# Kernel optimization log

Measured on AMD Instinct MI355X. Metric: run time of the kernel, lower is better.

Reference implementation:

```python
import jax, jax.numpy as jnp
import numpy as np

HEADS, CH = 10, 78          # GATv2Conv(78, 78, heads=10), concat=True -> 780
NUM_GRAPHS = 512            # from hardcoded (512 - 1) batch constant in forward
NEG_SLOPE = 0.2             # PyG GATv2 default


def _add_self_loops(edge_index, num_nodes):
    ar = jnp.arange(num_nodes, dtype=edge_index.dtype)
    loops = jnp.stack([ar, ar])
    return jnp.concatenate([edge_index, loops], axis=1)


def _gatv2_conv(x, edge_index, Wl, Wr, att_a, b_gat):
    # PyG GATv2Conv: e_ij = a^T LeakyReLU(W_l x_j + W_r x_i), softmax over j per i
    N = x.shape[0]
    ei = _add_self_loops(edge_index, N)
    src, dst = ei[0], ei[1]
    xl = (x @ Wl).reshape(N, HEADS, CH)  # source transform
    xr = (x @ Wr).reshape(N, HEADS, CH)  # target transform
    e = jax.nn.leaky_relu(xl[src] + xr[dst], NEG_SLOPE)      # [E, H, C]
    logits = jnp.einsum('ehc,hc->eh', e, att_a)              # [E, H]
    m = jax.ops.segment_max(logits, dst, num_segments=N)     # per-dst max
    p = jnp.exp(logits - m[dst])
    denom = jax.ops.segment_sum(p, dst, num_segments=N)
    alpha = p / denom[dst]                                   # [E, H]
    out = jax.ops.segment_sum(alpha[:, :, None] * xl[src], dst, num_segments=N)
    return out.reshape(N, HEADS * CH) + b_gat


def _gcn_conv(x, edge_index, W, b):
    # PyG GCNConv with self-loops and symmetric normalization
    N = x.shape[0]
    ei = _add_self_loops(edge_index, N)
    src, dst = ei[0], ei[1]
    deg = jax.ops.segment_sum(jnp.ones_like(dst, dtype=x.dtype), dst, num_segments=N)
    dinv = jnp.where(deg > 0, jax.lax.rsqrt(deg), 0.0)
    norm = dinv[src] * dinv[dst]                             # [E]
    h = x @ W
    return jax.ops.segment_sum(norm[:, None] * h[src], dst, num_segments=N) + b


def _pool_max_mean(x, batch):
    # global_max_pool and global_mean_pool over graph ids
    mx = jax.ops.segment_max(x, batch, num_segments=NUM_GRAPHS)
    mx = jnp.where(jnp.isfinite(mx), mx, 0.0)
    s = jax.ops.segment_sum(x, batch, num_segments=NUM_GRAPHS)
    cnt = jax.ops.segment_sum(jnp.ones((x.shape[0],), x.dtype), batch, num_segments=NUM_GRAPHS)
    mn = s / jnp.maximum(cnt, 1.0)[:, None]
    return jnp.concatenate([mx, mn], axis=1)


def setup_inputs() -> dict:
    key = jax.random.key(0)
    ks = jax.random.split(key, 13)
    N, E = 16384, 262144
    s = 0.05
    return {
        'x': jax.random.normal(ks[0], (N, 78), jnp.float32),
        'edge_index': jax.random.randint(ks[1], (2, E), 0, N, dtype=jnp.int32),
        'batch': jnp.sort(jax.random.randint(ks[2], (N,), 0, NUM_GRAPHS, dtype=jnp.int32)),
        'Wl': jax.random.normal(ks[3], (78, 780), jnp.float32) * s,
        'Wr': jax.random.normal(ks[4], (78, 780), jnp.float32) * s,
        'att_a': jax.random.normal(ks[5], (HEADS, CH), jnp.float32) * s,
        'b_gat': jax.random.normal(ks[6], (780,), jnp.float32) * s,
        'W_gcn': jax.random.normal(ks[7], (780, 780), jnp.float32) * s,
        'b_gcn': jax.random.normal(ks[8], (780,), jnp.float32) * s,
        'W_fc1': jax.random.normal(ks[9], (1560, 1500), jnp.float32) * s,
        'b_fc1': jax.random.normal(ks[10], (1500,), jnp.float32) * s,
        'W_fc2': jax.random.normal(ks[11], (1500, 128), jnp.float32) * s,
        'b_fc2': jax.random.normal(ks[12], (128,), jnp.float32) * s,
    }


def reference(x, edge_index, batch, Wl, Wr, att_a, b_gat, W_gcn, b_gcn,
              W_fc1, b_fc1, W_fc2, b_fc2):
    h = jax.nn.relu(_gatv2_conv(x, edge_index, Wl, Wr, att_a, b_gat))
    h = jax.nn.relu(_gcn_conv(h, edge_index, W_gcn, b_gcn))
    g = _pool_max_mean(h, batch)                 # [G, 1560]
    g = jax.nn.relu(g @ W_fc1 + b_fc1)           # fc_g1 (dropout is eval-mode identity)
    out = g @ W_fc2 + b_fc2                      # fc_g2 -> [G, 128]
    return out
```

## Files before the change

### kernel.cpp

```cpp
#include <hip/hip_runtime.h>
#include <hip/hip_bf16.h>
#include <math.h>
#include <stdio.h>

#define HEADS 10
#define CH 78
#define F 780
#define NGRAPH 512
#define NEG 0.2f
#define KPAD 832
#define NPAD 896
#define K1 128
#define N1 1560
#define N1PAD 1664
#define K2PAD 1600
#define N2PAD 1536

typedef __attribute__((ext_vector_type(8))) short short8;
typedef __attribute__((ext_vector_type(4))) float f32x4;
typedef __fp16 __attribute__((ext_vector_type(2))) h2;

__device__ inline void bf2unpack(unsigned int u, float& lo, float& hi) {
  union { unsigned int ui; float f; } a, b;
  a.ui = u << 16;
  b.ui = u & 0xffff0000u;
  lo = a.f; hi = b.f;
}

__global__ __launch_bounds__(256) void prep_k(const float* __restrict__ x,
                                              const float* __restrict__ Wl,
                                              const float* __restrict__ Wr,
                                              const float* __restrict__ Wgcn,
                                              const float* __restrict__ Wfc1,
                                              const float* __restrict__ Wfc2,
                                              const float* __restrict__ bfc2,
                                              __hip_bfloat16* __restrict__ xb,
                                              __hip_bfloat16* __restrict__ Wlrb,
                                              __hip_bfloat16* __restrict__ Wtb,
                                              __hip_bfloat16* __restrict__ Wfc1b,
                                              __hip_bfloat16* __restrict__ Wfc2b,
                                              float* __restrict__ outinit,
                                              int* __restrict__ counts, int Nn) {
  int i = blockIdx.x * 256 + threadIdx.x;
  int s0 = Nn * K1;
  int s1 = s0 + N1PAD * K1;
  int s2 = s1 + NPAD * KPAD;
  int s3 = s2 + N2PAD * K2PAD;
  int s4 = s3 + 128 * N2PAD;
  int s5 = s4 + NGRAPH * 128;
  int s6 = s5 + Nn;
  if (i < s0) {
    int row = i / K1, k = i - row * K1;
    xb[i] = __float2bfloat16((k < 78) ? x[(size_t)row * 78 + k] : 0.f);
  } else if (i < s1) {
    int j = i - s0;
    int n = j / K1, k = j - n * K1;
    float v = 0.f;
    if (k < 78 && n < N1) v = (n < F) ? Wl[(size_t)k * F + n] : Wr[(size_t)k * F + (n - F)];
    Wlrb[j] = __float2bfloat16(v);
  } else if (i < s2) {
    int j = i - s1;
    int n = j / KPAD, k = j - n * KPAD;
    float v = (n < F && k < F) ? Wgcn[(size_t)k * F + n] : 0.f;
    Wtb[j] = __float2bfloat16(v);
  } else if (i < s3) {
    int j = i - s2;
    int n = j / K2PAD, k = j - n * K2PAD;
    float v = (n < 1500 && k < 1560) ? Wfc1[(size_t)k * 1500 + n] : 0.f;
    Wfc1b[j] = __float2bfloat16(v);
  } else if (i < s4) {
    int j = i - s3;
    int n = j / N2PAD, k = j - n * N2PAD;
    float v = (k < 1500) ? Wfc2[(size_t)k * 128 + n] : 0.f;
    Wfc2b[j] = __float2bfloat16(v);
  } else if (i < s5) {
    int j = i - s4;
    outinit[j] = bfc2[j & 127];
  } else if (i < s6) {
    counts[i - s5] = 1;
  }
}

__device__ inline void gl_lds16(const unsigned short* g, unsigned short* l) {
  __builtin_amdgcn_global_load_lds(
      (const __attribute__((address_space(1))) unsigned int*)g,
      (__attribute__((address_space(3))) unsigned int*)l, 16, 0, 0);
}

#define MFMA_CORE64(A, Bt, lda, K)                                                \
  __shared__ unsigned short As[128 * 64];                                         \
  __shared__ unsigned short Bs[128 * 64];                                         \
  int tid = threadIdx.x;                                                          \
  int wave = tid >> 6, lane = tid & 63;                                           \
  int m0 = blockIdx.y * 128, n0 = blockIdx.x * 128;                               \
  int wr = (wave >> 1) * 64, wc = (wave & 1) * 64;                                \
  f32x4 acc[4][4];                                                                \
  _Pragma("unroll")                                                               \
  for (int i = 0; i < 4; ++i)                                                     \
    _Pragma("unroll")                                                             \
    for (int j = 0; j < 4; ++j) acc[i][j] = (f32x4){0.f, 0.f, 0.f, 0.f};          \
  int lrow = lane >> 3;                                                           \
  int lcol = (lane & 7) * 8;                                                      \
  const unsigned short* gA0 = A + (size_t)(m0 + wave * 32 + lrow) * lda + lcol;   \
  const unsigned short* gB0 = Bt + (size_t)(n0 + wave * 32 + lrow) * lda + lcol;  \
  unsigned short* lA = As + (wave * 32) * 64;                                     \
  unsigned short* lB = Bs + (wave * 32) * 64;                                     \
  int q8 = (lane >> 4) * 8;                                                       \
  int fr = lane & 15;                                                             \
  for (int k0 = 0; k0 < K; k0 += 64) {                                            \
    _Pragma("unroll")                                                             \
    for (int c = 0; c < 4; ++c) {                                                 \
      gl_lds16(gA0 + (size_t)(8 * c) * lda, lA + (8 * c) * 64);                   \
      gl_lds16(gB0 + (size_t)(8 * c) * lda, lB + (8 * c) * 64);                   \
    }                                                                             \
    gA0 += 64; gB0 += 64;                                                         \
    __syncthreads();                                                              \
    _Pragma("unroll")                                                             \
    for (int ks = 0; ks < 64; ks += 32) {                                         \
      short8 a[4], b[4];                                                          \
      _Pragma("unroll")                                                           \
      for (int i = 0; i < 4; ++i) a[i] = *(const short8*)&As[(wr + 16 * i + fr) * 64 + ks + q8]; \
      _Pragma("unroll")                                                           \
      for (int j = 0; j < 4; ++j) b[j] = *(const short8*)&Bs[(wc + 16 * j + fr) * 64 + ks + q8]; \
      _Pragma("unroll")                                                           \
      for (int i = 0; i < 4; ++i)                                                 \
        _Pragma("unroll")                                                         \
        for (int j = 0; j < 4; ++j)                                               \
          acc[i][j] = __builtin_amdgcn_mfma_f32_16x16x32_bf16(a[i], b[j], acc[i][j], 0, 0, 0); \
    }                                                                             \
    __syncthreads();                                                              \
  }                                                                               \
  int cq = (lane >> 4) * 4;

__global__ __launch_bounds__(256) void gemm_f16_dual_k(const unsigned short* __restrict__ A,
                                                       const unsigned short* __restrict__ Bt,
                                                       _Float16* __restrict__ Cl,
                                                       _Float16* __restrict__ Cr,
                                                       int M, int Ncols, int K, int lda) {
  MFMA_CORE64(A, Bt, lda, K)
#pragma unroll
  for (int i = 0; i < 4; ++i) {
#pragma unroll
    for (int j = 0; j < 4; ++j) {
      int col = n0 + wc + 16 * j + fr;
      if (col >= Ncols) continue;
      int rowb = m0 + wr + 16 * i + cq;
#pragma unroll
      for (int r = 0; r < 4; ++r) {
        int row = rowb + r;
        if (row >= M) continue;
        float v = acc[i][j][r];
        if (col < F) Cl[(size_t)row * F + col] = (_Float16)v;
        else         Cr[(size_t)row * F + (col - F)] = (_Float16)v;
      }
    }
  }
}

__global__ __launch_bounds__(256) void gemm_f16o_k(const unsigned short* __restrict__ A,
                                                   const unsigned short* __restrict__ Bt,
                                                   _Float16* __restrict__ C,
                                                   int M, int Ncols, int K, int lda) {
  MFMA_CORE64(A, Bt, lda, K)
#pragma unroll
  for (int i = 0; i < 4; ++i) {
#pragma unroll
    for (int j = 0; j < 4; ++j) {
      int col = n0 + wc + 16 * j + fr;
      if (col >= Ncols) continue;
      int rowb = m0 + wr + 16 * i + cq;
#pragma unroll
      for (int r = 0; r < 4; ++r) {
        int row = rowb + r;
        if (row < M) C[(size_t)row * Ncols + col] = (_Float16)acc[i][j][r];
      }
    }
  }
}

__global__ __launch_bounds__(256) void gemm_bf16_fc1_k(const unsigned short* __restrict__ A,
                                                       const unsigned short* __restrict__ Bt,
                                                       const float* __restrict__ bias,
                                                       __hip_bfloat16* __restrict__ C,
                                                       int M, int Nreal, int K, int lda) {
  MFMA_CORE64(A, Bt, lda, K)
#pragma unroll
  for (int i = 0; i < 4; ++i) {
#pragma unroll
    for (int j = 0; j < 4; ++j) {
      int col = n0 + wc + 16 * j + fr;
      int rowb = m0 + wr + 16 * i + cq;
#pragma unroll
      for (int r = 0; r < 4; ++r) {
        int row = rowb + r;
        if (row >= M) continue;
        float v = 0.f;
        if (col < Nreal) v = fmaxf(acc[i][j][r] + bias[col], 0.f);
        C[(size_t)row * N2PAD + col] = __float2bfloat16(v);
      }
    }
  }
}

__global__ __launch_bounds__(256) void gemm_bf16_fc2_k(const unsigned short* __restrict__ A,
                                                       const unsigned short* __restrict__ Bt,
                                                       float* C, int M, int kchunk) {
  const unsigned short* A2 = A + (size_t)blockIdx.z * kchunk;
  const unsigned short* B2 = Bt + (size_t)blockIdx.z * kchunk;
  MFMA_CORE64(A2, B2, N2PAD, kchunk)
#pragma unroll
  for (int i = 0; i < 4; ++i) {
#pragma unroll
    for (int j = 0; j < 4; ++j) {
      int col = n0 + wc + 16 * j + fr;
      int rowb = m0 + wr + 16 * i + cq;
#pragma unroll
      for (int r = 0; r < 4; ++r) {
        int row = rowb + r;
        if (row < M && col < 128) atomicAdd(&C[(size_t)row * 128 + col], acc[i][j][r]);
      }
    }
  }
}

__global__ void count_k(const int* __restrict__ dstv, int E, int* counts) {
  for (int e = blockIdx.x * blockDim.x + threadIdx.x; e < E; e += gridDim.x * blockDim.x)
    atomicAdd(&counts[dstv[e]], 1);
}
__global__ __launch_bounds__(256) void scan_k(const int* __restrict__ counts,
                                              int* __restrict__ row_start, int Nn) {
  __shared__ int part[256];
  int t = threadIdx.x;
  int chunk = (Nn + 255) / 256;
  int b0 = t * chunk, b1 = min(b0 + chunk, Nn);
  int s = 0;
  for (int i = b0; i < b1; ++i) s += counts[i];
  part[t] = s;
  __syncthreads();
  for (int off = 1; off < 256; off <<= 1) {
    int u = (t >= off) ? part[t - off] : 0;
    __syncthreads();
    part[t] += u;
    __syncthreads();
  }
  int run = part[t] - s;
  for (int i = b0; i < b1; ++i) { row_start[i] = run; run += counts[i]; }
  if (t == 255) row_start[Nn] = run;
}
__global__ void node_init_k(const int* __restrict__ row_start, int* cursor, int* csr_src,
                            float* dinv, int Nn) {
  int i = blockIdx.x * blockDim.x + threadIdx.x;
  if (i < Nn) {
    int p = row_start[i];
    csr_src[p] = i;
    cursor[i] = p + 1;
    dinv[i] = rsqrtf((float)(row_start[i + 1] - p));
  }
}
__global__ void scatter_k(const int* __restrict__ srcv, const int* __restrict__ dstv, int E,
                          int* cursor, int* csr_src) {
  for (int e = blockIdx.x * blockDim.x + threadIdx.x; e < E; e += gridDim.x * blockDim.x) {
    int pos = atomicAdd(&cursor[dstv[e]], 1);
    csr_src[pos] = srcv[e];
  }
}

#define GAT_EDGE(U0, U1)                                                       \
  { h2 x0 = __builtin_bit_cast(h2, U0);                                        \
    h2 x1 = __builtin_bit_cast(h2, U1);                                        \
    h2 v0 = x0 + xr0;                                                          \
    h2 v1 = x1 + xr1;                                                          \
    h2 l0 = __builtin_elementwise_max(v0, v0 * ns2);                           \
    h2 l1 = __builtin_elementwise_max(v1, v1 * ns2);                           \
    float p = __builtin_amdgcn_fdot2(l1, at1,                                  \
                __builtin_amdgcn_fdot2(l0, at0, 0.f, false), false);           \
    p += __shfl_xor(p, 16, 32);                                                \
    p += __shfl_xor(p, 8, 32);                                                 \
    p += __shfl_xor(p, 4, 32);                                                 \
    p += __shfl_xor(p, 2, 32);                                                 \
    p += __shfl_xor(p, 1, 32);                                                 \
    p = __expf(p);                                                             \
    denom += p;                                                                \
    h2 ph = __builtin_amdgcn_cvt_pkrtz(p, p);                                  \
    acc0 += ph * x0;                                                           \
    acc1 += ph * x1; }

__global__ __launch_bounds__(320) void gatv2_fused_k(const _Float16* __restrict__ xl,
                                                     const _Float16* __restrict__ xr,
                                                     const float* __restrict__ att,
                                                     const float* __restrict__ b_gat,
                                                     const int* __restrict__ row_start,
                                                     const int* __restrict__ csr_src,
                                                     __hip_bfloat16* __restrict__ h1out) {
  int dst = blockIdx.x;
  int t = threadIdx.x;
  int h = t >> 5, w = t & 31;
  int hb = h * CH;
  bool hasP1 = (w < 7);
  int c0 = hb + 2 * w;
  int c1 = hb + 64 + 2 * w;
  const h2 ns2 = {(__fp16)NEG, (__fp16)NEG};
  const unsigned short* xru = (const unsigned short*)xr + (size_t)dst * F;
  h2 xr0 = __builtin_bit_cast(h2, *(const unsigned int*)(xru + c0));
  unsigned int uxr1 = hasP1 ? *(const unsigned int*)(xru + c1) : 0u;
  h2 xr1 = __builtin_bit_cast(h2, uxr1);
  h2 at0 = __builtin_amdgcn_cvt_pkrtz(att[c0], att[c0 + 1]);
  h2 at1 = hasP1 ? __builtin_amdgcn_cvt_pkrtz(att[c1], att[c1 + 1])
                 : __builtin_amdgcn_cvt_pkrtz(0.f, 0.f);
  int r0 = row_start[dst], r1 = row_start[dst + 1];
  float denom = 0.f;
  h2 acc0 = {(__fp16)0, (__fp16)0};
  h2 acc1 = {(__fp16)0, (__fp16)0};
  const unsigned short* xlu = (const unsigned short*)xl;

  unsigned int uA0, uA1, uB0, uB1;
  {
    unsigned oA = (unsigned)csr_src[r0] * 780u;
    uA0 = *(const unsigned int*)(xlu + oA + c0);
    uA1 = hasP1 ? *(const unsigned int*)(xlu + oA + c1) : 0u;
    int jB = (r0 + 1 < r1) ? r0 + 1 : r0;
    unsigned oB = (unsigned)csr_src[jB] * 780u;
    uB0 = *(const unsigned int*)(xlu + oB + c0);
    uB1 = hasP1 ? *(const unsigned int*)(xlu + oB + c1) : 0u;
  }
  int j = r0;
#pragma unroll 2
  for (; j + 1 < r1; j += 2) {
    int j2 = j + 2; j2 = (j2 < r1) ? j2 : r0;
    int j3 = j + 3; j3 = (j3 < r1) ? j3 : r0;
    unsigned o2 = (unsigned)csr_src[j2] * 780u;
    unsigned o3 = (unsigned)csr_src[j3] * 780u;
    unsigned int uC0 = *(const unsigned int*)(xlu + o2 + c0);
    unsigned int uC1 = hasP1 ? *(const unsigned int*)(xlu + o2 + c1) : 0u;
    unsigned int uD0 = *(const unsigned int*)(xlu + o3 + c0);
    unsigned int uD1 = hasP1 ? *(const unsigned int*)(xlu + o3 + c1) : 0u;
    GAT_EDGE(uA0, uA1);
    GAT_EDGE(uB0, uB1);
    uA0 = uC0; uA1 = uC1;
    uB0 = uD0; uB1 = uD1;
  }
  if ((r1 - r0) & 1) GAT_EDGE(uA0, uA1);

  float inv = 1.f / denom;
  __hip_bfloat16* orow = h1out + (size_t)dst * KPAD;
  orow[c0] = __float2bfloat16(fmaxf((float)acc0.x * inv + b_gat[c0], 0.f));
  orow[c0 + 1] = __float2bfloat16(fmaxf((float)acc0.y * inv + b_gat[c0 + 1], 0.f));
  if (hasP1) {
    orow[c1] = __float2bfloat16(fmaxf((float)acc1.x * inv + b_gat[c1], 0.f));
    orow[c1 + 1] = __float2bfloat16(fmaxf((float)acc1.y * inv + b_gat[c1 + 1], 0.f));
  }
  if (t < KPAD - F) orow[F + t] = __float2bfloat16(0.f);
}

#define AGG_EDGE(U0, U1, NV)                                                   \
  { float nrm = di * (NV);                                                     \
    h2 nh = __builtin_amdgcn_cvt_pkrtz(nrm, nrm);                              \
    a0 += nh * __builtin_bit_cast(h2, U0);                                     \
    a1 += nh * __builtin_bit_cast(h2, U1); }

__global__ __launch_bounds__(320) void gcn_agg_k(const _Float16* __restrict__ hmat,
                                                 const float* __restrict__ bias,
                                                 const int* __restrict__ row_start,
                                                 const int* __restrict__ csr_src,
                                                 const float* __restrict__ dinv,
                                                 __hip_bfloat16* __restrict__ out) {
  int dst = blockIdx.x;
  int t = threadIdx.x;
  bool hasP1 = (t < 70);
  int c0 = 2 * t;
  int c1 = 640 + 2 * t;
  int r0 = row_start[dst], r1 = row_start[dst + 1];
  float di = dinv[dst];
  h2 a0 = {(__fp16)0, (__fp16)0};
  h2 a1 = {(__fp16)0, (__fp16)0};
  const unsigned short* hu = (const unsigned short*)hmat;

  unsigned int uA0, uA1, uB0, uB1;
  float nvA, nvB;
  {
    int sA = csr_src[r0];
    nvA = dinv[sA];
    unsigned oA = (unsigned)sA * 780u;
    uA0 = *(const unsigned int*)(hu + oA + c0);
    uA1 = hasP1 ? *(const unsigned int*)(hu + oA + c1) : 0u;
    int jB = (r0 + 1 < r1) ? r0 + 1 : r0;
    int sB = csr_src[jB];
    nvB = dinv[sB];
    unsigned oB = (unsigned)sB * 780u;
    uB0 = *(const unsigned int*)(hu + oB + c0);
    uB1 = hasP1 ? *(const unsigned int*)(hu + oB + c1) : 0u;
  }
  int j = r0;
#pragma unroll 2
  for (; j + 1 < r1; j += 2) {
    int j2 = j + 2; j2 = (j2 < r1) ? j2 : r0;
    int j3 = j + 3; j3 = (j3 < r1) ? j3 : r0;
    int s2 = csr_src[j2];
    int s3 = csr_src[j3];
    float nv2 = dinv[s2];
    float nv3 = dinv[s3];
    unsigned o2 = (unsigned)s2 * 780u;
    unsigned o3 = (unsigned)s3 * 780u;
    unsigned int uC0 = *(const unsigned int*)(hu + o2 + c0);
    unsigned int uC1 = hasP1 ? *(const unsigned int*)(hu + o2 + c1) : 0u;
    unsigned int uD0 = *(const unsigned int*)(hu + o3 + c0);
    unsigned int uD1 = hasP1 ? *(const unsigned int*)(hu + o3 + c1) : 0u;
    AGG_EDGE(uA0, uA1, nvA);
    AGG_EDGE(uB0, uB1, nvB);
    uA0 = uC0; uA1 = uC1; nvA = nv2;
    uB0 = uD0; uB1 = uD1; nvB = nv3;
  }
  if ((r1 - r0) & 1) AGG_EDGE(uA0, uA1, nvA);

  __hip_bfloat16* o = out + (size_t)dst * F;
  o[c0] = __float2bfloat16(fmaxf((float)a0.x + bias[c0], 0.f));
  o[c0 + 1] = __float2bfloat16(fmaxf((float)a0.y + bias[c0 + 1], 0.f));
  if (hasP1) {
    o[c1] = __float2bfloat16(fmaxf((float)a1.x + bias[c1], 0.f));
    o[c1 + 1] = __float2bfloat16(fmaxf((float)a1.y + bias[c1 + 1], 0.f));
  }
}

__global__ __launch_bounds__(320) void pool_k(const __hip_bfloat16* __restrict__ hmat,
                                              const int* __restrict__ batch,
                                              __hip_bfloat16* __restrict__ pooled, int Nn) {
  int g = blockIdx.x;
  int t = threadIdx.x;
  __shared__ int lo_s, hi_s;
  if (t == 0) {
    int lo = 0, hi = Nn;
    while (lo < hi) { int mid = (lo + hi) >> 1; if (batch[mid] < g) lo = mid + 1; else hi = mid; }
    lo_s = lo;
    int lo2 = lo, hi2 = Nn;
    while (lo2 < hi2) { int mid = (lo2 + hi2) >> 1; if (batch[mid] < g + 1) lo2 = mid + 1; else hi2 = mid; }
    hi_s = lo2;
  }
  __syncthreads();
  int lo = lo_s, hi = hi_s, cnt = hi - lo;
  bool hasP1 = (t < 70);
  int c0 = 2 * t;
  int c1 = 640 + 2 * t;
  float m0a = -1e30f, m0b = -1e30f, m1a = -1e30f, m1b = -1e30f;
  float s0a = 0.f, s0b = 0.f, s1a = 0.f, s1b = 0.f;
  const unsigned short* hu = (const unsigned short*)hmat;
  for (int n = lo; n < hi; ++n) {
    const unsigned short* hp = hu + (size_t)n * F;
    unsigned int u0 = *(const unsigned int*)(hp + c0);
    float v0x, v0y;
    bf2unpack(u0, v0x, v0y);
    m0a = fmaxf(m0a, v0x); s0a += v0x;
    m0b = fmaxf(m0b, v0y); s0b += v0y;
    if (hasP1) {
      unsigned int u1 = *(const unsigned int*)(hp + c1);
      float v1x, v1y;
      bf2unpack(u1, v1x, v1y);
      m1a = fmaxf(m1a, v1x); s1a += v1x;
      m1b = fmaxf(m1b, v1y); s1b += v1y;
    }
  }
  float inv = 1.f / (float)(cnt > 0 ? cnt : 1);
  __hip_bfloat16* o = pooled + (size_t)g * K2PAD;
  o[c0] = __float2bfloat16(cnt ? m0a : 0.f);
  o[c0 + 1] = __float2bfloat16(cnt ? m0b : 0.f);
  o[780 + c0] = __float2bfloat16(s0a * inv);
  o[780 + c0 + 1] = __float2bfloat16(s0b * inv);
  if (hasP1) {
    o[c1] = __float2bfloat16(cnt ? m1a : 0.f);
    o[c1 + 1] = __float2bfloat16(cnt ? m1b : 0.f);
    o[780 + c1] = __float2bfloat16(s1a * inv);
    o[780 + c1 + 1] = __float2bfloat16(s1b * inv);
  }
  if (t < K2PAD - 1560) o[1560 + t] = __float2bfloat16(0.f);
}

extern "C" void kernel_launch(void* const* d_in, const int* in_sizes, int n_in,
                              void* d_out, int out_size, void* d_ws, size_t ws_size,
                              hipStream_t stream) {
  const float* x     = (const float*)d_in[0];
  const int*   ei    = (const int*)d_in[1];
  const int*   batch = (const int*)d_in[2];
  const float* Wl    = (const float*)d_in[3];
  const float* Wr    = (const float*)d_in[4];
  const float* att   = (const float*)d_in[5];
  const float* b_gat = (const float*)d_in[6];
  const float* W_gcn = (const float*)d_in[7];
  const float* b_gcn = (const float*)d_in[8];
  const float* W_fc1 = (const float*)d_in[9];
  const float* b_fc1 = (const float*)d_in[10];
  const float* W_fc2 = (const float*)d_in[11];
  const float* b_fc2 = (const float*)d_in[12];
  float* out = (float*)d_out;

  int Nn = in_sizes[0] / 78;
  int E  = in_sizes[1] / 2;
  int EP = E + Nn;
  const int* srcv = ei;
  const int* dstv = ei + E;

  char* wsb = (char*)d_ws;
  size_t NB = (size_t)Nn * F;
  _Float16* xrh = (_Float16*)wsb;
  __hip_bfloat16* aggbf = (__hip_bfloat16*)wsb;
  wsb += NB * sizeof(_Float16);
  _Float16* bufH = (_Float16*)wsb;
  wsb += NB * sizeof(_Float16);
  __hip_bfloat16* h1bf = (__hip_bfloat16*)wsb;
  wsb += (size_t)Nn * KPAD * sizeof(__hip_bfloat16);
  __hip_bfloat16* xbf = (__hip_bfloat16*)wsb;
  wsb += (size_t)Nn * K1 * sizeof(__hip_bfloat16);
  __hip_bfloat16* Wlrb = (__hip_bfloat16*)wsb;
  wsb += (size_t)N1PAD * K1 * sizeof(__hip_bfloat16);
  __hip_bfloat16* Wtb = (__hip_bfloat16*)wsb;
  wsb += (size_t)NPAD * KPAD * sizeof(__hip_bfloat16);
  __hip_bfloat16* Wfc1b = (__hip_bfloat16*)wsb;
  wsb += (size_t)N2PAD * K2PAD * sizeof(__hip_bfloat16);
  __hip_bfloat16* Wfc2b = (__hip_bfloat16*)wsb;
  wsb += (size_t)128 * N2PAD * sizeof(__hip_bfloat16);
  __hip_bfloat16* pooledb = (__hip_bfloat16*)wsb;
  wsb += (size_t)NGRAPH * K2PAD * sizeof(__hip_bfloat16);
  __hip_bfloat16* g1b = (__hip_bfloat16*)wsb;
  wsb += (size_t)NGRAPH * N2PAD * sizeof(__hip_bfloat16);
  int* csr_src = (int*)wsb;      wsb += (size_t)EP * sizeof(int);
  int* counts = (int*)wsb;       wsb += (size_t)Nn * sizeof(int);
  int* row_start = (int*)wsb;    wsb += (size_t)(Nn + 1) * sizeof(int);
  int* cursor = (int*)wsb;       wsb += (size_t)Nn * sizeof(int);
  float* dinv = (float*)wsb;     wsb += (size_t)Nn * sizeof(float);
  size_t need = (size_t)(wsb - (char*)d_ws);
  if (need > ws_size) {
    fprintf(stderr, "kernel_launch: ws too small: need %zu have %zu\n", need, ws_size);
  }

  dim3 blk(256);

  int prep_total = Nn * K1 + N1PAD * K1 + NPAD * KPAD + N2PAD * K2PAD + 128 * N2PAD
                 + NGRAPH * 128 + Nn;
  prep_k<<<(prep_total + 255) / 256, 256, 0, stream>>>(x, Wl, Wr, W_gcn, W_fc1, W_fc2, b_fc2,
                                                       xbf, Wlrb, Wtb, Wfc1b, Wfc2b,
                                                       out, counts, Nn);

  count_k<<<512, 256, 0, stream>>>(dstv, E, counts);
  scan_k<<<1, 256, 0, stream>>>(counts, row_start, Nn);
  node_init_k<<<(Nn + 255) / 256, 256, 0, stream>>>(row_start, cursor, csr_src, dinv, Nn);
  scatter_k<<<512, 256, 0, stream>>>(srcv, dstv, E, cursor, csr_src);

  dim3 g1grid(N1PAD / 128, Nn / 128);
  gemm_f16_dual_k<<<g1grid, blk, 0, stream>>>((const unsigned short*)xbf,
                                              (const unsigned short*)Wlrb,
                                              bufH, xrh, Nn, N1, K1, K1);

  gatv2_fused_k<<<Nn, 320, 0, stream>>>(bufH, xrh, att, b_gat, row_start, csr_src, h1bf);

  dim3 g2grid(NPAD / 128, Nn / 128);
  gemm_f16o_k<<<g2grid, blk, 0, stream>>>((const unsigned short*)h1bf,
                                          (const unsigned short*)Wtb,
                                          bufH, Nn, F, KPAD, KPAD);

  gcn_agg_k<<<Nn, 320, 0, stream>>>(bufH, b_gcn, row_start, csr_src, dinv, aggbf);

  pool_k<<<NGRAPH, 320, 0, stream>>>(aggbf, batch, pooledb, Nn);

  dim3 fc1grid(N2PAD / 128, NGRAPH / 128);
  gemm_bf16_fc1_k<<<fc1grid, blk, 0, stream>>>((const unsigned short*)pooledb,
                                               (const unsigned short*)Wfc1b,
                                               b_fc1, g1b, NGRAPH, 1500, K2PAD, K2PAD);

  dim3 fc2grid(1, NGRAPH / 128, 6);
  gemm_bf16_fc2_k<<<fc2grid, blk, 0, stream>>>((const unsigned short*)g1b,
                                               (const unsigned short*)Wfc2b,
                                               out, NGRAPH, 256);
}
```

Measured before the change: 504.1 us.

## Pad GAT features per head, vectorize gathers, deepen prefetch, DPP reductions

```diff
diff --git a/kernel.cpp b/kernel.cpp
--- a/kernel.cpp
+++ b/kernel.cpp
@@ -6,6 +6,7 @@
 #define HEADS 10
 #define CH 78
 #define F 780
+#define FP 800
 #define NGRAPH 512
 #define NEG 0.2f
 #define KPAD 832
@@ -26,6 +27,10 @@
   b.ui = u & 0xffff0000u;
   lo = a.f; hi = b.f;
 }
+
+#define DPP_ADDF(v, ctrl)                                                      \
+  ((v) + __builtin_bit_cast(float, __builtin_amdgcn_update_dpp(                \
+             0, __builtin_bit_cast(int, (v)), ctrl, 0xF, 0xF, true)))
 
 __global__ __launch_bounds__(256) void prep_k(const float* __restrict__ x,
                                               const float* __restrict__ Wl,
@@ -144,14 +149,16 @@
     for (int j = 0; j < 4; ++j) {
       int col = n0 + wc + 16 * j + fr;
       if (col >= Ncols) continue;
+      int c = (col < F) ? col : col - F;
+      int head = c / 78;
+      int pcol = head * 80 + (c - head * 78);
+      _Float16* Cp = (col < F) ? Cl : Cr;
       int rowb = m0 + wr + 16 * i + cq;
 #pragma unroll
       for (int r = 0; r < 4; ++r) {
         int row = rowb + r;
         if (row >= M) continue;
-        float v = acc[i][j][r];
-        if (col < F) Cl[(size_t)row * F + col] = (_Float16)v;
-        else         Cr[(size_t)row * F + (col - F)] = (_Float16)v;
+        Cp[(size_t)row * FP + pcol] = (_Float16)acc[i][j][r];
       }
     }
   }
@@ -265,20 +272,20 @@
   }
 }
 
-#define GAT_EDGE(U0, U1)                                                       \
-  { h2 x0 = __builtin_bit_cast(h2, U0);                                        \
-    h2 x1 = __builtin_bit_cast(h2, U1);                                        \
+#define GAT_EDGE(U)                                                            \
+  { h2 x0 = __builtin_bit_cast(h2, (U).x);                                     \
+    h2 x1 = __builtin_bit_cast(h2, (U).y);                                     \
     h2 v0 = x0 + xr0;                                                          \
     h2 v1 = x1 + xr1;                                                          \
     h2 l0 = __builtin_elementwise_max(v0, v0 * ns2);                           \
     h2 l1 = __builtin_elementwise_max(v1, v1 * ns2);                           \
     float p = __builtin_amdgcn_fdot2(l1, at1,                                  \
                 __builtin_amdgcn_fdot2(l0, at0, 0.f, false), false);           \
+    p = DPP_ADDF(p, 0xB1);                                                     \
+    p = DPP_ADDF(p, 0x4E);                                                     \
+    p = DPP_ADDF(p, 0x141);                                                    \
+    p = DPP_ADDF(p, 0x140);                                                    \
     p += __shfl_xor(p, 16, 32);                                                \
-    p += __shfl_xor(p, 8, 32);                                                 \
-    p += __shfl_xor(p, 4, 32);                                                 \
-    p += __shfl_xor(p, 2, 32);                                                 \
-    p += __shfl_xor(p, 1, 32);                                                 \
     p = __expf(p);                                                             \
     denom += p;                                                                \
     h2 ph = __builtin_amdgcn_cvt_pkrtz(p, p);                                  \
@@ -295,70 +302,71 @@
   int dst = blockIdx.x;
   int t = threadIdx.x;
   int h = t >> 5, w = t & 31;
-  int hb = h * CH;
-  bool hasP1 = (w < 7);
-  int c0 = hb + 2 * w;
-  int c1 = hb + 64 + 2 * w;
+  int lq = (w < 19) ? w : 19;
+  int qoff = h * 80 + 4 * lq;
   const h2 ns2 = {(__fp16)NEG, (__fp16)NEG};
-  const unsigned short* xru = (const unsigned short*)xr + (size_t)dst * F;
-  h2 xr0 = __builtin_bit_cast(h2, *(const unsigned int*)(xru + c0));
-  unsigned int uxr1 = hasP1 ? *(const unsigned int*)(xru + c1) : 0u;
-  h2 xr1 = __builtin_bit_cast(h2, uxr1);
-  h2 at0 = __builtin_amdgcn_cvt_pkrtz(att[c0], att[c0 + 1]);
-  h2 at1 = hasP1 ? __builtin_amdgcn_cvt_pkrtz(att[c1], att[c1 + 1])
-                 : __builtin_amdgcn_cvt_pkrtz(0.f, 0.f);
+  const unsigned short* xru = (const unsigned short*)xr;
+  uint2 uxr = *(const uint2*)(xru + (size_t)dst * FP + qoff);
+  h2 xr0 = __builtin_bit_cast(h2, uxr.x);
+  h2 xr1 = __builtin_bit_cast(h2, uxr.y);
+  float a0 = 0.f, a1 = 0.f, a2 = 0.f, a3 = 0.f;
+  int cb = h * 78 + 4 * w;
+  if (w < 20) {
+    a0 = att[cb]; a1 = att[cb + 1];
+    if (w < 19) { a2 = att[cb + 2]; a3 = att[cb + 3]; }
+  }
+  h2 at0 = __builtin_amdgcn_cvt_pkrtz(a0, a1);
+  h2 at1 = __builtin_amdgcn_cvt_pkrtz(a2, a3);
   int r0 = row_start[dst], r1 = row_start[dst + 1];
   float denom = 0.f;
   h2 acc0 = {(__fp16)0, (__fp16)0};
   h2 acc1 = {(__fp16)0, (__fp16)0};
   const unsigned short* xlu = (const unsigned short*)xl;
 
-  unsigned int uA0, uA1, uB0, uB1;
+#define GAT_LD(jj) (*(const uint2*)(xlu + (size_t)((unsigned)csr_src[jj]) * FP + qoff))
+  uint2 e0, e1, e2, e3, e4, e5;
   {
-    unsigned oA = (unsigned)csr_src[r0] * 780u;
-    uA0 = *(const unsigned int*)(xlu + oA + c0);
-    uA1 = hasP1 ? *(const unsigned int*)(xlu + oA + c1) : 0u;
-    int jB = (r0 + 1 < r1) ? r0 + 1 : r0;
-    unsigned oB = (unsigned)csr_src[jB] * 780u;
-    uB0 = *(const unsigned int*)(xlu + oB + c0);
-    uB1 = hasP1 ? *(const unsigned int*)(xlu + oB + c1) : 0u;
+    int i1 = (r0 + 1 < r1) ? r0 + 1 : r0;
+    int i2 = (r0 + 2 < r1) ? r0 + 2 : r0;
+    int i3 = (r0 + 3 < r1) ? r0 + 3 : r0;
+    int i4 = (r0 + 4 < r1) ? r0 + 4 : r0;
+    int i5 = (r0 + 5 < r1) ? r0 + 5 : r0;
+    e0 = GAT_LD(r0); e1 = GAT_LD(i1); e2 = GAT_LD(i2);
+    e3 = GAT_LD(i3); e4 = GAT_LD(i4); e5 = GAT_LD(i5);
   }
   int j = r0;
-#pragma unroll 2
   for (; j + 1 < r1; j += 2) {
-    int j2 = j + 2; j2 = (j2 < r1) ? j2 : r0;
-    int j3 = j + 3; j3 = (j3 < r1) ? j3 : r0;
-    unsigned o2 = (unsigned)csr_src[j2] * 780u;
-    unsigned o3 = (unsigned)csr_src[j3] * 780u;
-    unsigned int uC0 = *(const unsigned int*)(xlu + o2 + c0);
-    unsigned int uC1 = hasP1 ? *(const unsigned int*)(xlu + o2 + c1) : 0u;
-    unsigned int uD0 = *(const unsigned int*)(xlu + o3 + c0);
-    unsigned int uD1 = hasP1 ? *(const unsigned int*)(xlu + o3 + c1) : 0u;
-    GAT_EDGE(uA0, uA1);
-    GAT_EDGE(uB0, uB1);
-    uA0 = uC0; uA1 = uC1;
-    uB0 = uD0; uB1 = uD1;
-  }
-  if ((r1 - r0) & 1) GAT_EDGE(uA0, uA1);
+    int j6 = j + 6; j6 = (j6 < r1) ? j6 : r0;
+    int j7 = j + 7; j7 = (j7 < r1) ? j7 : r0;
+    uint2 f6 = GAT_LD(j6);
+    uint2 f7 = GAT_LD(j7);
+    GAT_EDGE(e0);
+    GAT_EDGE(e1);
+    e0 = e2; e1 = e3; e2 = e4; e3 = e5; e4 = f6; e5 = f7;
+  }
+  if ((r1 - r0) & 1) GAT_EDGE(e0);
+#undef GAT_LD
 
   float inv = 1.f / denom;
   __hip_bfloat16* orow = h1out + (size_t)dst * KPAD;
-  orow[c0] = __float2bfloat16(fmaxf((float)acc0.x * inv + b_gat[c0], 0.f));
-  orow[c0 + 1] = __float2bfloat16(fmaxf((float)acc0.y * inv + b_gat[c0 + 1], 0.f));
-  if (hasP1) {
-    orow[c1] = __float2bfloat16(fmaxf((float)acc1.x * inv + b_gat[c1], 0.f));
-    orow[c1 + 1] = __float2bfloat16(fmaxf((float)acc1.y * inv + b_gat[c1 + 1], 0.f));
+  if (w < 20) {
+    orow[cb] = __float2bfloat16(fmaxf((float)acc0.x * inv + b_gat[cb], 0.f));
+    orow[cb + 1] = __float2bfloat16(fmaxf((float)acc0.y * inv + b_gat[cb + 1], 0.f));
+    if (w < 19) {
+      orow[cb + 2] = __float2bfloat16(fmaxf((float)acc1.x * inv + b_gat[cb + 2], 0.f));
+      orow[cb + 3] = __float2bfloat16(fmaxf((float)acc1.y * inv + b_gat[cb + 3], 0.f));
+    }
   }
   if (t < KPAD - F) orow[F + t] = __float2bfloat16(0.f);
 }
 
-#define AGG_EDGE(U0, U1, NV)                                                   \
+#define AGG_EDGE(U, NV)                                                        \
   { float nrm = di * (NV);                                                     \
     h2 nh = __builtin_amdgcn_cvt_pkrtz(nrm, nrm);                              \
-    a0 += nh * __builtin_bit_cast(h2, U0);                                     \
-    a1 += nh * __builtin_bit_cast(h2, U1); }
-
-__global__ __launch_bounds__(320) void gcn_agg_k(const _Float16* __restrict__ hmat,
+    a0 += nh * __builtin_bit_cast(h2, (U).x);                                  \
+    a1 += nh * __builtin_bit_cast(h2, (U).y); }
+
+__global__ __launch_bounds__(256) void gcn_agg_k(const _Float16* __restrict__ hmat,
                                                  const float* __restrict__ bias,
                                                  const int* __restrict__ row_start,
                                                  const int* __restrict__ csr_src,
@@ -366,58 +374,55 @@
                                                  __hip_bfloat16* __restrict__ out) {
   int dst = blockIdx.x;
   int t = threadIdx.x;
-  bool hasP1 = (t < 70);
-  int c0 = 2 * t;
-  int c1 = 640 + 2 * t;
+  int tq = (t < 195) ? t : 194;
+  int q = 4 * tq;
   int r0 = row_start[dst], r1 = row_start[dst + 1];
   float di = dinv[dst];
   h2 a0 = {(__fp16)0, (__fp16)0};
   h2 a1 = {(__fp16)0, (__fp16)0};
   const unsigned short* hu = (const unsigned short*)hmat;
 
-  unsigned int uA0, uA1, uB0, uB1;
-  float nvA, nvB;
+#define AGG_LD(ss) (*(const uint2*)(hu + (size_t)(unsigned)(ss) * F + q))
+  uint2 e0, e1, e2, e3, e4, e5;
+  float n0v, n1v, n2v, n3v, n4v, n5v;
   {
-    int sA = csr_src[r0];
-    nvA = dinv[sA];
-    unsigned oA = (unsigned)sA * 780u;
-    uA0 = *(const unsigned int*)(hu + oA + c0);
-    uA1 = hasP1 ? *(const unsigned int*)(hu + oA + c1) : 0u;
-    int jB = (r0 + 1 < r1) ? r0 + 1 : r0;
-    int sB = csr_src[jB];
-    nvB = dinv[sB];
-    unsigned oB = (unsigned)sB * 780u;
-    uB0 = *(const unsigned int*)(hu + oB + c0);
-    uB1 = hasP1 ? *(const unsigned int*)(hu + oB + c1) : 0u;
+    int i1 = (r0 + 1 < r1) ? r0 + 1 : r0;
+    int i2 = (r0 + 2 < r1) ? r0 + 2 : r0;
+    int i3 = (r0 + 3 < r1) ? r0 + 3 : r0;
+    int i4 = (r0 + 4 < r1) ? r0 + 4 : r0;
+    int i5 = (r0 + 5 < r1) ? r0 + 5 : r0;
+    int s0 = csr_src[r0], s1 = csr_src[i1], s2 = csr_src[i2];
+    int s3 = csr_src[i3], s4 = csr_src[i4], s5 = csr_src[i5];
+    n0v = dinv[s0]; n1v = dinv[s1]; n2v = dinv[s2];
+    n3v = dinv[s3]; n4v = dinv[s4]; n5v = dinv[s5];
+    e0 = AGG_LD(s0); e1 = AGG_LD(s1); e2 = AGG_LD(s2);
+    e3 = AGG_LD(s3); e4 = AGG_LD(s4); e5 = AGG_LD(s5);
   }
   int j = r0;
-#pragma unroll 2
   for (; j + 1 < r1; j += 2) {
-    int j2 = j + 2; j2 = (j2 < r1) ? j2 : r0;
-    int j3 = j + 3; j3 = (j3 < r1) ? j3 : r0;
-    int s2 = csr_src[j2];
-    int s3 = csr_src[j3];
-    float nv2 = dinv[s2];
-    float nv3 = dinv[s3];
-    unsigned o2 = (unsigned)s2 * 780u;
-    unsigned o3 = (unsigned)s3 * 780u;
-    unsigned int uC0 = *(const unsigned int*)(hu + o2 + c0);
-    unsigned int uC1 = hasP1 ? *(const unsigned int*)(hu + o2 + c1) : 0u;
-    unsigned int uD0 = *(const unsigned int*)(hu + o3 + c0);
-    unsigned int uD1 = hasP1 ? *(const unsigned int*)(hu + o3 + c1) : 0u;
-    AGG_EDGE(uA0, uA1, nvA);
-    AGG_EDGE(uB0, uB1, nvB);
-    uA0 = uC0; uA1 = uC1; nvA = nv2;
-    uB0 = uD0; uB1 = uD1; nvB = nv3;
-  }
-  if ((r1 - r0) & 1) AGG_EDGE(uA0, uA1, nvA);
-
-  __hip_bfloat16* o = out + (size_t)dst * F;
-  o[c0] = __float2bfloat16(fmaxf((float)a0.x + bias[c0], 0.f));
-  o[c0 + 1] = __float2bfloat16(fmaxf((float)a0.y + bias[c0 + 1], 0.f));
-  if (hasP1) {
-    o[c1] = __float2bfloat16(fmaxf((float)a1.x + bias[c1], 0.f));
-    o[c1 + 1] = __float2bfloat16(fmaxf((float)a1.y + bias[c1 + 1], 0.f));
+    int j6 = j + 6; j6 = (j6 < r1) ? j6 : r0;
+    int j7 = j + 7; j7 = (j7 < r1) ? j7 : r0;
+    int s6 = csr_src[j6];
+    int s7 = csr_src[j7];
+    float n6v = dinv[s6];
+    float n7v = dinv[s7];
+    uint2 f6 = AGG_LD(s6);
+    uint2 f7 = AGG_LD(s7);
+    AGG_EDGE(e0, n0v);
+    AGG_EDGE(e1, n1v);
+    e0 = e2; n0v = n2v; e1 = e3; n1v = n3v;
+    e2 = e4; n2v = n4v; e3 = e5; n3v = n5v;
+    e4 = f6; n4v = n6v; e5 = f7; n5v = n7v;
+  }
+  if ((r1 - r0) & 1) AGG_EDGE(e0, n0v);
+#undef AGG_LD
+
+  if (t < 195) {
+    __hip_bfloat16* o = out + (size_t)dst * F + q;
+    o[0] = __float2bfloat16(fmaxf((float)a0.x + bias[q], 0.f));
+    o[1] = __float2bfloat16(fmaxf((float)a0.y + bias[q + 1], 0.f));
+    o[2] = __float2bfloat16(fmaxf((float)a1.x + bias[q + 2], 0.f));
+    o[3] = __float2bfloat16(fmaxf((float)a1.y + bias[q + 3], 0.f));
   }
 }
 
@@ -498,12 +503,12 @@
   const int* dstv = ei + E;
 
   char* wsb = (char*)d_ws;
-  size_t NB = (size_t)Nn * F;
+  size_t NBP = (size_t)Nn * FP;
   _Float16* xrh = (_Float16*)wsb;
   __hip_bfloat16* aggbf = (__hip_bfloat16*)wsb;
-  wsb += NB * sizeof(_Float16);
+  wsb += NBP * sizeof(_Float16);
   _Float16* bufH = (_Float16*)wsb;
-  wsb += NB * sizeof(_Float16);
+  wsb += NBP * sizeof(_Float16);
   __hip_bfloat16* h1bf = (__hip_bfloat16*)wsb;
   wsb += (size_t)Nn * KPAD * sizeof(__hip_bfloat16);
   __hip_bfloat16* xbf = (__hip_bfloat16*)wsb;
@@ -555,7 +560,7 @@
                                           (const unsigned short*)Wtb,
                                           bufH, Nn, F, KPAD, KPAD);
 
-  gcn_agg_k<<<Nn, 320, 0, stream>>>(bufH, b_gcn, row_start, csr_src, dinv, aggbf);
+  gcn_agg_k<<<Nn, 256, 0, stream>>>(bufH, b_gcn, row_start, csr_src, dinv, aggbf);
 
   pool_k<<<NGRAPH, 320, 0, stream>>>(aggbf, batch, pooledb, Nn);
 
```

Result: no change. 501.4 us (-0.5%).
